# Kernel optimization log

Hardware: AMD Instinct MI355X
Metric: run time of the kernel (lower is better)

The kernel has to match this reference:

```python
import jax, jax.numpy as jnp
import numpy as np

B, S, D = 2, 2048, 768
H = 12
DK = D // H  # 64; dim_q = dim_k = dim_v
DFF = 3072
EPS = 1e-5


def layer_norm(x, w, b):
    mu = jnp.mean(x, axis=-1, keepdims=True)
    var = jnp.var(x, axis=-1, keepdims=True)
    return (x - mu) * jax.lax.rsqrt(var + EPS) * w + b


def setup_inputs() -> dict:
    key = jax.random.key(0)
    ks = jax.random.split(key, 12)
    s = 0.02
    return {
        "src": jax.random.normal(ks[0], (B, S, D), dtype=jnp.float32),
        # per-head projections stacked over heads: [H, D, DK]
        "Wq": jax.random.normal(ks[1], (H, D, DK), dtype=jnp.float32) * s,
        "bq": jnp.zeros((H, DK), dtype=jnp.float32),
        "Wk": jax.random.normal(ks[2], (H, D, DK), dtype=jnp.float32) * s,
        "bk": jnp.zeros((H, DK), dtype=jnp.float32),
        "Wv": jax.random.normal(ks[3], (H, D, DK), dtype=jnp.float32) * s,
        "bv": jnp.zeros((H, DK), dtype=jnp.float32),
        # output projection: [H*DK, D]
        "Wo": jax.random.normal(ks[4], (H * DK, D), dtype=jnp.float32) * s,
        "bo": jnp.zeros((D,), dtype=jnp.float32),
        "ln1_w": jnp.ones((D,), dtype=jnp.float32),
        "ln1_b": jnp.zeros((D,), dtype=jnp.float32),
        "W1": jax.random.normal(ks[5], (D, DFF), dtype=jnp.float32) * s,
        "b1": jnp.zeros((DFF,), dtype=jnp.float32),
        "W2": jax.random.normal(ks[6], (DFF, D), dtype=jnp.float32) * s,
        "b2": jnp.zeros((D,), dtype=jnp.float32),
        "ln2_w": jnp.ones((D,), dtype=jnp.float32),
        "ln2_b": jnp.zeros((D,), dtype=jnp.float32),
    }


def reference(src, Wq, bq, Wk, bk, Wv, bv, Wo, bo, ln1_w, ln1_b,
              W1, b1, W2, b2, ln2_w, ln2_b):
    # per-head q/k/v projections, batched over heads via einsum
    q = jnp.einsum('bsd,hdk->bhsk', src, Wq) + bq[None, :, None, :]
    k = jnp.einsum('bsd,hdk->bhsk', src, Wk) + bk[None, :, None, :]
    v = jnp.einsum('bsd,hdk->bhsk', src, Wv) + bv[None, :, None, :]
    scale = jnp.asarray(DK, src.dtype) ** 0.5
    scores = jnp.einsum('bhsk,bhtk->bhst', q, k) / scale  # [B,H,S,S]
    attn = jax.nn.softmax(scores, axis=-1)
    ctx = jnp.einsum('bhst,bhtk->bhsk', attn, v)
    # concat heads along feature dim (matches torch.cat over head outputs)
    ctx = ctx.transpose(0, 2, 1, 3).reshape(src.shape[0], src.shape[1], H * DK)
    attn_out = ctx @ Wo + bo
    x = layer_norm(src + attn_out, ln1_w, ln1_b)
    ff = jax.nn.relu(x @ W1 + b1) @ W2 + b2
    return layer_norm(x + ff, ln2_w, ln2_b)
```

## Files before the change

### kernel.cpp

```cpp
#include <hip/hip_runtime.h>
#include <hip/hip_bf16.h>

#define S_LEN 2048
#define DMODEL 768
#define NHEAD 12
#define DKH 64
#define DFF_K 3072
#define MROWS 4096

typedef __attribute__((ext_vector_type(8))) short bf16x8;
typedef __attribute__((ext_vector_type(8))) unsigned short us8;
typedef __attribute__((ext_vector_type(4))) float f32x4;

__device__ __forceinline__ float bfu2f(unsigned short u) {
  return __uint_as_float(((unsigned int)u) << 16);
}
__device__ __forceinline__ unsigned short f2bfu(float f) {
  __hip_bfloat16 h = __float2bfloat16(f);
  return *reinterpret_cast<unsigned short*>(&h);
}

__global__ __launch_bounds__(256) void convert_kernel(
    const float* __restrict__ in, unsigned short* __restrict__ out, int n4)
{
  const int i = blockIdx.x * 256 + threadIdx.x;
  if (i < n4) {
    float4 v = *(const float4*)(in + (size_t)i * 4);
    ushort4 o;
    o.x = f2bfu(v.x); o.y = f2bfu(v.y); o.z = f2bfu(v.z); o.w = f2bfu(v.w);
    *(ushort4*)(out + (size_t)i * 4) = o;
  }
}

__device__ __forceinline__ void transpose_conv_body(
    const float* in, unsigned short* out, int R, int Ctot, int head,
    int bx, int by, int tid)
{
  __shared__ float t[64][68];
  const int r0 = bx * 64;
  const int c0 = by * 64;
  const float* ib;
  int ld;
  if (head) { ib = in + (size_t)by * R * 64; ld = 64; }
  else      { ib = in + c0;                  ld = Ctot; }
  const int lr = tid >> 4;
  const int lc = (tid & 15) << 2;

#pragma unroll
  for (int rr = 0; rr < 4; ++rr) {
    const int row = rr * 16 + lr;
    float4 v = *(const float4*)(ib + (size_t)(r0 + row) * ld + lc);
    t[row][lc + 0] = v.x; t[row][lc + 1] = v.y;
    t[row][lc + 2] = v.z; t[row][lc + 3] = v.w;
  }
  __syncthreads();
#pragma unroll
  for (int rr = 0; rr < 4; ++rr) {
    const int oc = rr * 16 + lr;
    ushort4 o;
    o.x = f2bfu(t[lc + 0][oc]); o.y = f2bfu(t[lc + 1][oc]);
    o.z = f2bfu(t[lc + 2][oc]); o.w = f2bfu(t[lc + 3][oc]);
    *(ushort4*)(out + (size_t)(c0 + oc) * R + r0 + lc) = o;
  }
}

__global__ __launch_bounds__(256) void transpose_conv_kernel(
    const float* __restrict__ in, unsigned short* __restrict__ out,
    int R, int Ctot, int head)
{
  transpose_conv_body(in, out, R, Ctot, head, blockIdx.x, blockIdx.y, threadIdx.x);
}

__global__ __launch_bounds__(256) void transpose_conv4_kernel(
    const float* __restrict__ i0, const float* __restrict__ i1,
    const float* __restrict__ i2, const float* __restrict__ i3,
    unsigned short* __restrict__ o0, unsigned short* __restrict__ o1,
    unsigned short* __restrict__ o2, unsigned short* __restrict__ o3)
{
  const int z = blockIdx.z;
  const float* in = (z == 0) ? i0 : (z == 1) ? i1 : (z == 2) ? i2 : i3;
  unsigned short* out = (z == 0) ? o0 : (z == 1) ? o1 : (z == 2) ? o2 : o3;
  transpose_conv_body(in, out, DMODEL, DMODEL, (z < 3) ? 1 : 0,
                      blockIdx.x, blockIdx.y, threadIdx.x);
}

__global__ __launch_bounds__(256) void mfma_gemm_kernel(
    const unsigned short* __restrict__ A,
    const unsigned short* __restrict__ BT,
    const float* __restrict__ bias,
    unsigned short* __restrict__ C,
    int K, int N, int relu, int klen, size_t out_stride)
{
  __shared__ unsigned short As[128][40];
  __shared__ unsigned short Bs[128][40];

  const int tid  = threadIdx.x;
  const int wid  = tid >> 6;
  const int lane = tid & 63;
  const int ml   = lane & 15;
  const int quad = lane >> 4;
  const int wm   = (wid & 1) * 64;
  const int wn   = (wid >> 1) * 64;
  const int row0 = blockIdx.x * 128;
  const int col0 = blockIdx.y * 128;
  const int zed  = blockIdx.z;
  const int kb0  = zed * klen;

  const int sr = tid >> 2;
  const int sk = (tid & 3) << 3;

  f32x4 acc[4][4];
#pragma unroll
  for (int i = 0; i < 4; ++i)
#pragma unroll
    for (int j = 0; j < 4; ++j)
#pragma unroll
      for (int r = 0; r < 4; ++r) acc[i][j][r] = 0.f;

  for (int k0 = kb0; k0 < kb0 + klen; k0 += 32) {
    us8 a0 = *(const us8*)(A + (size_t)(row0 + sr) * K + k0 + sk);
    us8 a1 = *(const us8*)(A + (size_t)(row0 + sr + 64) * K + k0 + sk);
    us8 b0 = *(const us8*)(BT + (size_t)(col0 + sr) * K + k0 + sk);
    us8 b1 = *(const us8*)(BT + (size_t)(col0 + sr + 64) * K + k0 + sk);
    *(us8*)&As[sr][sk]      = a0;
    *(us8*)&As[sr + 64][sk] = a1;
    *(us8*)&Bs[sr][sk]      = b0;
    *(us8*)&Bs[sr + 64][sk] = b1;
    __syncthreads();

    bf16x8 af[4], bfr[4];
#pragma unroll
    for (int i = 0; i < 4; ++i)
      af[i] = *(const bf16x8*)&As[wm + i * 16 + ml][quad << 3];
#pragma unroll
    for (int j = 0; j < 4; ++j)
      bfr[j] = *(const bf16x8*)&Bs[wn + j * 16 + ml][quad << 3];
#pragma unroll
    for (int i = 0; i < 4; ++i)
#pragma unroll
      for (int j = 0; j < 4; ++j)
        acc[i][j] = __builtin_amdgcn_mfma_f32_16x16x32_bf16(
            af[i], bfr[j], acc[i][j], 0, 0, 0);
    __syncthreads();
  }

  unsigned short* Cz = C + (size_t)zed * out_stride;
#pragma unroll
  for (int j = 0; j < 4; ++j) {
    const int col = col0 + wn + j * 16 + ml;
    const float bb = (zed == 0) ? bias[col] : 0.f;
#pragma unroll
    for (int i = 0; i < 4; ++i) {
      const int r0g = row0 + wm + i * 16 + (quad << 2);
#pragma unroll
      for (int r = 0; r < 4; ++r) {
        float v = acc[i][j][r] + bb;
        if (relu) v = fmaxf(v, 0.f);
        Cz[(size_t)(r0g + r) * N + col] = f2bfu(v);
      }
    }
  }
}

__global__ __launch_bounds__(256) void qkv_gemm_kernel(
    const unsigned short* __restrict__ A,
    const unsigned short* __restrict__ W0, const unsigned short* __restrict__ W1,
    const unsigned short* __restrict__ W2,
    const float* __restrict__ bq, const float* __restrict__ bk,
    const float* __restrict__ bv,
    unsigned short* __restrict__ C0, unsigned short* __restrict__ C1,
    unsigned short* __restrict__ C2)
{
  __shared__ unsigned short As[128][40];
  __shared__ unsigned short Bs[128][40];
  const int z = blockIdx.z;
  const unsigned short* BT = (z == 0) ? W0 : (z == 1) ? W1 : W2;
  const float* bias = (z == 0) ? bq : (z == 1) ? bk : bv;
  unsigned short* C = (z == 0) ? C0 : (z == 1) ? C1 : C2;
  const int K = DMODEL, N = DMODEL;

  const int tid  = threadIdx.x;
  const int wid  = tid >> 6;
  const int lane = tid & 63;
  const int ml   = lane & 15;
  const int quad = lane >> 4;
  const int wm   = (wid & 1) * 64;
  const int wn   = (wid >> 1) * 64;
  const int row0 = blockIdx.x * 128;
  const int col0 = blockIdx.y * 128;
  const int sr = tid >> 2;
  const int sk = (tid & 3) << 3;

  f32x4 acc[4][4];
#pragma unroll
  for (int i = 0; i < 4; ++i)
#pragma unroll
    for (int j = 0; j < 4; ++j)
#pragma unroll
      for (int r = 0; r < 4; ++r) acc[i][j][r] = 0.f;

  for (int k0 = 0; k0 < K; k0 += 32) {
    us8 a0 = *(const us8*)(A + (size_t)(row0 + sr) * K + k0 + sk);
    us8 a1 = *(const us8*)(A + (size_t)(row0 + sr + 64) * K + k0 + sk);
    us8 b0 = *(const us8*)(BT + (size_t)(col0 + sr) * K + k0 + sk);
    us8 b1 = *(const us8*)(BT + (size_t)(col0 + sr + 64) * K + k0 + sk);
    *(us8*)&As[sr][sk]      = a0;
    *(us8*)&As[sr + 64][sk] = a1;
    *(us8*)&Bs[sr][sk]      = b0;
    *(us8*)&Bs[sr + 64][sk] = b1;
    __syncthreads();
    bf16x8 af[4], bfr[4];
#pragma unroll
    for (int i = 0; i < 4; ++i)
      af[i] = *(const bf16x8*)&As[wm + i * 16 + ml][quad << 3];
#pragma unroll
    for (int j = 0; j < 4; ++j)
      bfr[j] = *(const bf16x8*)&Bs[wn + j * 16 + ml][quad << 3];
#pragma unroll
    for (int i = 0; i < 4; ++i)
#pragma unroll
      for (int j = 0; j < 4; ++j)
        acc[i][j] = __builtin_amdgcn_mfma_f32_16x16x32_bf16(
            af[i], bfr[j], acc[i][j], 0, 0, 0);
    __syncthreads();
  }

#pragma unroll
  for (int j = 0; j < 4; ++j) {
    const int col = col0 + wn + j * 16 + ml;
    const float bb = bias[col];
#pragma unroll
    for (int i = 0; i < 4; ++i) {
      const int r0g = row0 + wm + i * 16 + (quad << 2);
      if (z == 2) {
        const int bb_ = r0g >> 11, s = r0g & 2047;
        const int hh = col >> 6, dd = col & 63;
        ushort4 o;
        o.x = f2bfu(acc[i][j][0] + bb); o.y = f2bfu(acc[i][j][1] + bb);
        o.z = f2bfu(acc[i][j][2] + bb); o.w = f2bfu(acc[i][j][3] + bb);
        *(ushort4*)(C + ((size_t)((bb_ * NHEAD + hh) * DKH + dd)) * S_LEN + s) = o;
      } else {
#pragma unroll
        for (int r = 0; r < 4; ++r)
          C[(size_t)(r0g + r) * N + col] = f2bfu(acc[i][j][r] + bb);
      }
    }
  }
}

#define FATS 72
#define SCL2E 0.1803368822f
__global__ __launch_bounds__(256) void flash_attn_mfma(
    const unsigned short* __restrict__ Q,
    const unsigned short* __restrict__ K,
    const unsigned short* __restrict__ VT,
    unsigned short* __restrict__ O)
{
  __shared__ unsigned short Ks[64][FATS];
  __shared__ unsigned short Vs[64][FATS];
  __shared__ unsigned short QP[4][16][FATS];

  const int tid  = threadIdx.x;
  const int wid  = tid >> 6;
  const int lane = tid & 63;
  const int ml   = lane & 15;
  const int quad = lane >> 4;
  const int h    = blockIdx.x, b = blockIdx.y;
  const int q0   = blockIdx.z * 64;

  const size_t qkbase = ((size_t)b * S_LEN) * DMODEL + (size_t)h * DKH;
  const size_t vtbase = ((size_t)(b * NHEAD + h)) * DKH * S_LEN;

  const int sr = tid >> 2;
  const int sc = (tid & 3) << 4;

  {
    const unsigned short* qp = Q + qkbase + (size_t)(q0 + sr) * DMODEL + sc;
    *(us8*)&QP[sr >> 4][sr & 15][sc]     = *(const us8*)qp;
    *(us8*)&QP[sr >> 4][sr & 15][sc + 8] = *(const us8*)(qp + 8);
  }
  bf16x8 qf[2];
  qf[0] = *(const bf16x8*)&QP[wid][ml][quad << 3];
  qf[1] = *(const bf16x8*)&QP[wid][ml][32 + (quad << 3)];

  float lsum = 0.f;
  f32x4 oacc[4];
#pragma unroll
  for (int dt = 0; dt < 4; ++dt)
#pragma unroll
    for (int r = 0; r < 4; ++r) oacc[dt][r] = 0.f;

  for (int kt = 0; kt < S_LEN; kt += 64) {
    __syncthreads();
    {
      const unsigned short* kp = K + qkbase + (size_t)(kt + sr) * DMODEL + sc;
      *(us8*)&Ks[sr][sc]     = *(const us8*)kp;
      *(us8*)&Ks[sr][sc + 8] = *(const us8*)(kp + 8);
      const unsigned short* vp = VT + vtbase + (size_t)sr * S_LEN + kt + sc;
      *(us8*)&Vs[sr][sc]     = *(const us8*)vp;
      *(us8*)&Vs[sr][sc + 8] = *(const us8*)(vp + 8);
    }
    __syncthreads();

    f32x4 sacc[4];
#pragma unroll
    for (int mt = 0; mt < 4; ++mt)
#pragma unroll
      for (int r = 0; r < 4; ++r) sacc[mt][r] = 0.f;
#pragma unroll
    for (int mt = 0; mt < 4; ++mt) {
      bf16x8 kf0 = *(const bf16x8*)&Ks[mt * 16 + ml][quad << 3];
      bf16x8 kf1 = *(const bf16x8*)&Ks[mt * 16 + ml][32 + (quad << 3)];
      sacc[mt] = __builtin_amdgcn_mfma_f32_16x16x32_bf16(kf0, qf[0], sacc[mt], 0, 0, 0);
      sacc[mt] = __builtin_amdgcn_mfma_f32_16x16x32_bf16(kf1, qf[1], sacc[mt], 0, 0, 0);
    }

    float p[4][4];
#pragma unroll
    for (int mt2 = 0; mt2 < 4; ++mt2)
#pragma unroll
      for (int r = 0; r < 4; ++r) {
        const float e = exp2f(sacc[mt2][r] * SCL2E);
        p[mt2][r] = e;
        lsum += e;
      }

#pragma unroll
    for (int mt2 = 0; mt2 < 4; ++mt2) {
      ushort4 o;
      o.x = f2bfu(p[mt2][0]); o.y = f2bfu(p[mt2][1]);
      o.z = f2bfu(p[mt2][2]); o.w = f2bfu(p[mt2][3]);
      *(ushort4*)&QP[wid][ml][mt2 * 16 + (quad << 2)] = o;
    }
    bf16x8 pf0 = *(const bf16x8*)&QP[wid][ml][quad << 3];
    bf16x8 pf1 = *(const bf16x8*)&QP[wid][ml][32 + (quad << 3)];

#pragma unroll
    for (int dt = 0; dt < 4; ++dt) {
      bf16x8 vf0 = *(const bf16x8*)&Vs[dt * 16 + ml][quad << 3];
      bf16x8 vf1 = *(const bf16x8*)&Vs[dt * 16 + ml][32 + (quad << 3)];
      oacc[dt] = __builtin_amdgcn_mfma_f32_16x16x32_bf16(vf0, pf0, oacc[dt], 0, 0, 0);
      oacc[dt] = __builtin_amdgcn_mfma_f32_16x16x32_bf16(vf1, pf1, oacc[dt], 0, 0, 0);
    }
  }

  lsum += __shfl_xor(lsum, 16);
  lsum += __shfl_xor(lsum, 32);
  const float inv = 1.f / lsum;
  const int qrow = q0 + wid * 16 + ml;
#pragma unroll
  for (int dt = 0; dt < 4; ++dt)
#pragma unroll
    for (int r = 0; r < 4; ++r)
      O[qkbase + (size_t)qrow * DMODEL + dt * 16 + (quad << 2) + r] =
          f2bfu(oacc[dt][r] * inv);
}

__global__ __launch_bounds__(256) void add_ln_kernel(
    const void* __restrict__ X, const void* __restrict__ Y,
    const void* __restrict__ Y2,
    const float* __restrict__ w, const float* __restrict__ bvec,
    void* __restrict__ out, int xbf, int ybf, int obf)
{
  __shared__ float buf[DMODEL];
  __shared__ float rbuf[8];
  const int tid  = threadIdx.x;
  const int lane = tid & 63, wv = tid >> 6;
  const size_t base = (size_t)blockIdx.x * DMODEL;

  float s = 0.f, s2 = 0.f;
#pragma unroll
  for (int j = tid; j < DMODEL; j += 256) {
    float xv = xbf ? bfu2f(((const unsigned short*)X)[base + j])
                   : ((const float*)X)[base + j];
    float yv = ybf ? bfu2f(((const unsigned short*)Y)[base + j])
                   : ((const float*)Y)[base + j];
    float v = xv + yv;
    if (Y2) v += ybf ? bfu2f(((const unsigned short*)Y2)[base + j])
                     : ((const float*)Y2)[base + j];
    buf[j] = v; s += v; s2 += v * v;
  }
#pragma unroll
  for (int o = 32; o; o >>= 1) { s += __shfl_xor(s, o); s2 += __shfl_xor(s2, o); }
  if (lane == 0) { rbuf[wv] = s; rbuf[4 + wv] = s2; }
  __syncthreads();
  const float S  = rbuf[0] + rbuf[1] + rbuf[2] + rbuf[3];
  const float S2 = rbuf[4] + rbuf[5] + rbuf[6] + rbuf[7];
  const float mean = S * (1.f / (float)DMODEL);
  const float var  = S2 * (1.f / (float)DMODEL) - mean * mean;
  const float rstd = rsqrtf(var + 1e-5f);
#pragma unroll
  for (int j = tid; j < DMODEL; j += 256) {
    float v = (buf[j] - mean) * rstd * w[j] + bvec[j];
    if (obf) ((unsigned short*)out)[base + j] = f2bfu(v);
    else     ((float*)out)[base + j] = v;
  }
}

extern "C" void kernel_launch(void* const* d_in, const int* in_sizes, int n_in,
                              void* d_out, int out_size, void* d_ws, size_t ws_size,
                              hipStream_t stream) {
  const float* src  = (const float*)d_in[0];
  const float* Wq   = (const float*)d_in[1];
  const float* bq   = (const float*)d_in[2];
  const float* Wk   = (const float*)d_in[3];
  const float* bk   = (const float*)d_in[4];
  const float* Wv   = (const float*)d_in[5];
  const float* bv   = (const float*)d_in[6];
  const float* Wo   = (const float*)d_in[7];
  const float* bo   = (const float*)d_in[8];
  const float* ln1w = (const float*)d_in[9];
  const float* ln1b = (const float*)d_in[10];
  const float* W1   = (const float*)d_in[11];
  const float* b1   = (const float*)d_in[12];
  const float* W2   = (const float*)d_in[13];
  const float* b2   = (const float*)d_in[14];
  const float* ln2w = (const float*)d_in[15];
  const float* ln2b = (const float*)d_in[16];
  (void)ws_size; (void)in_sizes; (void)n_in; (void)out_size;

  unsigned short* p = (unsigned short*)d_ws;
  const size_t SEG = (size_t)MROWS * DMODEL;
  unsigned short* srcb = p; p += SEG;
  unsigned short* qb   = p; p += SEG;
  unsigned short* kb_  = p; p += SEG;
  unsigned short* vbT  = p; p += SEG;
  unsigned short* ctx  = p; p += SEG;
  unsigned short* ff   = p; p += (size_t)MROWS * DFF_K;
  unsigned short* wqt  = p; p += (size_t)DMODEL * DMODEL;
  unsigned short* wkt  = p; p += (size_t)DMODEL * DMODEL;
  unsigned short* wvt  = p; p += (size_t)DMODEL * DMODEL;
  unsigned short* wot  = p; p += (size_t)DMODEL * DMODEL;
  unsigned short* w1t  = p; p += (size_t)DMODEL * DFF_K;
  unsigned short* w2t  = p; p += (size_t)DMODEL * DFF_K;
  unsigned short* x1 = kb_;

  dim3 blk(256);

  convert_kernel<<<dim3(SEG / 1024), blk, 0, stream>>>(src, srcb, (int)(SEG / 4));
  transpose_conv4_kernel<<<dim3(12, 12, 4), blk, 0, stream>>>(
      Wq, Wk, Wv, Wo, wqt, wkt, wvt, wot);
  transpose_conv_kernel<<<dim3(12, 48), blk, 0, stream>>>(W1, w1t, DMODEL, DFF_K, 0);
  transpose_conv_kernel<<<dim3(48, 12), blk, 0, stream>>>(W2, w2t, DFF_K, DMODEL, 0);

  dim3 gqkv(MROWS / 128, DMODEL / 128, 3);
  qkv_gemm_kernel<<<gqkv, blk, 0, stream>>>(srcb, wqt, wkt, wvt, bq, bk, bv,
                                            qb, kb_, vbT);

  dim3 ga(NHEAD, 2, S_LEN / 64);
  flash_attn_mfma<<<ga, blk, 0, stream>>>(qb, kb_, vbT, ctx);

  dim3 gWo(MROWS / 128, DMODEL / 128, 2);
  mfma_gemm_kernel<<<gWo, blk, 0, stream>>>(ctx, wot, bo, qb,
                                            DMODEL, DMODEL, 0, DMODEL / 2, 2 * SEG);

  add_ln_kernel<<<dim3(MROWS), blk, 0, stream>>>(srcb, qb, vbT,
                                                 ln1w, ln1b, x1, 1, 1, 1);

  dim3 gF1(MROWS / 128, DFF_K / 128, 1);
  mfma_gemm_kernel<<<gF1, blk, 0, stream>>>(x1, w1t, b1, ff,
                                            DMODEL, DFF_K, 1, DMODEL, 0);

  dim3 gW2(MROWS / 128, DMODEL / 128, 2);
  mfma_gemm_kernel<<<gW2, blk, 0, stream>>>(ff, w2t, b2, qb,
                                            DFF_K, DMODEL, 0, DFF_K / 2, 2 * SEG);

  add_ln_kernel<<<dim3(MROWS), blk, 0, stream>>>(x1, qb, vbT,
                                                 ln2w, ln2b, (float*)d_out, 1, 1, 0);
}
```

Baseline: 335.8 us.

## Prefetch next K-tile into registers and use narrower N tiles for small GEMMs

The GEMM and flash-attention kernels now issue the global loads for the next K/V or K-slice tile into registers before running the MFMAs on the current tile, so memory latency overlaps with compute. The GEMM kernel is templated on its N-tile width, and the QKV, Wo and W2 GEMMs switch to 64-wide column tiles, doubling their block counts to fill the GPU's compute units better. This costs extra live registers for the prefetched data, and the narrower tiles reuse each loaded A tile across fewer columns.

```diff
diff --git a/kernel.cpp b/kernel.cpp
--- a/kernel.cpp
+++ b/kernel.cpp
@@ -84,6 +84,7 @@
                       blockIdx.x, blockIdx.y, threadIdx.x);
 }
 
+template<int BN>
 __global__ __launch_bounds__(256) void mfma_gemm_kernel(
     const unsigned short* __restrict__ A,
     const unsigned short* __restrict__ BT,
@@ -91,8 +92,10 @@
     unsigned short* __restrict__ C,
     int K, int N, int relu, int klen, size_t out_stride)
 {
+  constexpr int WN = (BN == 128) ? 64 : 32;
+  constexpr int NJ = WN / 16;
   __shared__ unsigned short As[128][40];
-  __shared__ unsigned short Bs[128][40];
+  __shared__ unsigned short Bs[BN][40];
 
   const int tid  = threadIdx.x;
   const int wid  = tid >> 6;
@@ -100,45 +103,61 @@
   const int ml   = lane & 15;
   const int quad = lane >> 4;
   const int wm   = (wid & 1) * 64;
-  const int wn   = (wid >> 1) * 64;
+  const int wn   = (wid >> 1) * WN;
   const int row0 = blockIdx.x * 128;
-  const int col0 = blockIdx.y * 128;
+  const int col0 = blockIdx.y * BN;
   const int zed  = blockIdx.z;
   const int kb0  = zed * klen;
+  const int kend = kb0 + klen;
 
   const int sr = tid >> 2;
   const int sk = (tid & 3) << 3;
 
-  f32x4 acc[4][4];
+  const unsigned short* pA0 = A  + (size_t)(row0 + sr) * K + sk;
+  const unsigned short* pA1 = A  + (size_t)(row0 + sr + 64) * K + sk;
+  const unsigned short* pB0 = BT + (size_t)(col0 + sr) * K + sk;
+  const unsigned short* pB1 = BT + (size_t)(col0 + sr + 64) * K + sk;
+
+  f32x4 acc[4][NJ];
 #pragma unroll
   for (int i = 0; i < 4; ++i)
 #pragma unroll
-    for (int j = 0; j < 4; ++j)
+    for (int j = 0; j < NJ; ++j)
 #pragma unroll
       for (int r = 0; r < 4; ++r) acc[i][j][r] = 0.f;
 
-  for (int k0 = kb0; k0 < kb0 + klen; k0 += 32) {
-    us8 a0 = *(const us8*)(A + (size_t)(row0 + sr) * K + k0 + sk);
-    us8 a1 = *(const us8*)(A + (size_t)(row0 + sr + 64) * K + k0 + sk);
-    us8 b0 = *(const us8*)(BT + (size_t)(col0 + sr) * K + k0 + sk);
-    us8 b1 = *(const us8*)(BT + (size_t)(col0 + sr + 64) * K + k0 + sk);
-    *(us8*)&As[sr][sk]      = a0;
-    *(us8*)&As[sr + 64][sk] = a1;
-    *(us8*)&Bs[sr][sk]      = b0;
-    *(us8*)&Bs[sr + 64][sk] = b1;
+  us8 ra0 = *(const us8*)(pA0 + kb0);
+  us8 ra1 = *(const us8*)(pA1 + kb0);
+  us8 rb0 = *(const us8*)(pB0 + kb0);
+  us8 rb1;
+  if (BN == 128) rb1 = *(const us8*)(pB1 + kb0);
+
+  for (int k0 = kb0; k0 < kend; k0 += 32) {
+    *(us8*)&As[sr][sk]      = ra0;
+    *(us8*)&As[sr + 64][sk] = ra1;
+    *(us8*)&Bs[sr][sk]      = rb0;
+    if (BN == 128) *(us8*)&Bs[sr + 64][sk] = rb1;
     __syncthreads();
 
-    bf16x8 af[4], bfr[4];
+    const int kn = k0 + 32;
+    if (kn < kend) {
+      ra0 = *(const us8*)(pA0 + kn);
+      ra1 = *(const us8*)(pA1 + kn);
+      rb0 = *(const us8*)(pB0 + kn);
+      if (BN == 128) rb1 = *(const us8*)(pB1 + kn);
+    }
+
+    bf16x8 af[4], bfr[NJ];
 #pragma unroll
     for (int i = 0; i < 4; ++i)
       af[i] = *(const bf16x8*)&As[wm + i * 16 + ml][quad << 3];
 #pragma unroll
-    for (int j = 0; j < 4; ++j)
+    for (int j = 0; j < NJ; ++j)
       bfr[j] = *(const bf16x8*)&Bs[wn + j * 16 + ml][quad << 3];
 #pragma unroll
     for (int i = 0; i < 4; ++i)
 #pragma unroll
-      for (int j = 0; j < 4; ++j)
+      for (int j = 0; j < NJ; ++j)
         acc[i][j] = __builtin_amdgcn_mfma_f32_16x16x32_bf16(
             af[i], bfr[j], acc[i][j], 0, 0, 0);
     __syncthreads();
@@ -146,7 +165,7 @@
 
   unsigned short* Cz = C + (size_t)zed * out_stride;
 #pragma unroll
-  for (int j = 0; j < 4; ++j) {
+  for (int j = 0; j < NJ; ++j) {
     const int col = col0 + wn + j * 16 + ml;
     const float bb = (zed == 0) ? bias[col] : 0.f;
 #pragma unroll
@@ -172,7 +191,7 @@
     unsigned short* __restrict__ C2)
 {
   __shared__ unsigned short As[128][40];
-  __shared__ unsigned short Bs[128][40];
+  __shared__ unsigned short Bs[64][40];
   const int z = blockIdx.z;
   const unsigned short* BT = (z == 0) ? W0 : (z == 1) ? W1 : W2;
   const float* bias = (z == 0) ? bq : (z == 1) ? bk : bv;
@@ -185,48 +204,59 @@
   const int ml   = lane & 15;
   const int quad = lane >> 4;
   const int wm   = (wid & 1) * 64;
-  const int wn   = (wid >> 1) * 64;
+  const int wn   = (wid >> 1) * 32;
   const int row0 = blockIdx.x * 128;
-  const int col0 = blockIdx.y * 128;
+  const int col0 = blockIdx.y * 64;
   const int sr = tid >> 2;
   const int sk = (tid & 3) << 3;
 
-  f32x4 acc[4][4];
+  const unsigned short* pA0 = A  + (size_t)(row0 + sr) * K + sk;
+  const unsigned short* pA1 = A  + (size_t)(row0 + sr + 64) * K + sk;
+  const unsigned short* pB0 = BT + (size_t)(col0 + sr) * K + sk;
+
+  f32x4 acc[4][2];
 #pragma unroll
   for (int i = 0; i < 4; ++i)
 #pragma unroll
-    for (int j = 0; j < 4; ++j)
+    for (int j = 0; j < 2; ++j)
 #pragma unroll
       for (int r = 0; r < 4; ++r) acc[i][j][r] = 0.f;
 
+  us8 ra0 = *(const us8*)pA0;
+  us8 ra1 = *(const us8*)pA1;
+  us8 rb0 = *(const us8*)pB0;
+
   for (int k0 = 0; k0 < K; k0 += 32) {
-    us8 a0 = *(const us8*)(A + (size_t)(row0 + sr) * K + k0 + sk);
-    us8 a1 = *(const us8*)(A + (size_t)(row0 + sr + 64) * K + k0 + sk);
-    us8 b0 = *(const us8*)(BT + (size_t)(col0 + sr) * K + k0 + sk);
-    us8 b1 = *(const us8*)(BT + (size_t)(col0 + sr + 64) * K + k0 + sk);
-    *(us8*)&As[sr][sk]      = a0;
-    *(us8*)&As[sr + 64][sk] = a1;
-    *(us8*)&Bs[sr][sk]      = b0;
-    *(us8*)&Bs[sr + 64][sk] = b1;
+    *(us8*)&As[sr][sk]      = ra0;
+    *(us8*)&As[sr + 64][sk] = ra1;
+    *(us8*)&Bs[sr][sk]      = rb0;
     __syncthreads();
-    bf16x8 af[4], bfr[4];
+
+    const int kn = k0 + 32;
+    if (kn < K) {
+      ra0 = *(const us8*)(pA0 + kn);
+      ra1 = *(const us8*)(pA1 + kn);
+      rb0 = *(const us8*)(pB0 + kn);
+    }
+
+    bf16x8 af[4], bfr[2];
 #pragma unroll
     for (int i = 0; i < 4; ++i)
       af[i] = *(const bf16x8*)&As[wm + i * 16 + ml][quad << 3];
 #pragma unroll
-    for (int j = 0; j < 4; ++j)
+    for (int j = 0; j < 2; ++j)
       bfr[j] = *(const bf16x8*)&Bs[wn + j * 16 + ml][quad << 3];
 #pragma unroll
     for (int i = 0; i < 4; ++i)
 #pragma unroll
-      for (int j = 0; j < 4; ++j)
+      for (int j = 0; j < 2; ++j)
         acc[i][j] = __builtin_amdgcn_mfma_f32_16x16x32_bf16(
             af[i], bfr[j], acc[i][j], 0, 0, 0);
     __syncthreads();
   }
 
 #pragma unroll
-  for (int j = 0; j < 4; ++j) {
+  for (int j = 0; j < 2; ++j) {
     const int col = col0 + wn + j * 16 + ml;
     const float bb = bias[col];
 #pragma unroll
@@ -283,6 +313,9 @@
   qf[0] = *(const bf16x8*)&QP[wid][ml][quad << 3];
   qf[1] = *(const bf16x8*)&QP[wid][ml][32 + (quad << 3)];
 
+  const unsigned short* pK = K + qkbase + (size_t)sr * DMODEL + sc;
+  const unsigned short* pV = VT + vtbase + (size_t)sr * S_LEN + sc;
+
   float lsum = 0.f;
   f32x4 oacc[4];
 #pragma unroll
@@ -290,17 +323,26 @@
 #pragma unroll
     for (int r = 0; r < 4; ++r) oacc[dt][r] = 0.f;
 
+  us8 rk0 = *(const us8*)(pK);
+  us8 rk1 = *(const us8*)(pK + 8);
+  us8 rv0 = *(const us8*)(pV);
+  us8 rv1 = *(const us8*)(pV + 8);
+
   for (int kt = 0; kt < S_LEN; kt += 64) {
     __syncthreads();
-    {
-      const unsigned short* kp = K + qkbase + (size_t)(kt + sr) * DMODEL + sc;
-      *(us8*)&Ks[sr][sc]     = *(const us8*)kp;
-      *(us8*)&Ks[sr][sc + 8] = *(const us8*)(kp + 8);
-      const unsigned short* vp = VT + vtbase + (size_t)sr * S_LEN + kt + sc;
-      *(us8*)&Vs[sr][sc]     = *(const us8*)vp;
-      *(us8*)&Vs[sr][sc + 8] = *(const us8*)(vp + 8);
-    }
+    *(us8*)&Ks[sr][sc]     = rk0;
+    *(us8*)&Ks[sr][sc + 8] = rk1;
+    *(us8*)&Vs[sr][sc]     = rv0;
+    *(us8*)&Vs[sr][sc + 8] = rv1;
     __syncthreads();
+
+    const int ktn = kt + 64;
+    if (ktn < S_LEN) {
+      rk0 = *(const us8*)(pK + (size_t)ktn * DMODEL);
+      rk1 = *(const us8*)(pK + (size_t)ktn * DMODEL + 8);
+      rv0 = *(const us8*)(pV + ktn);
+      rv1 = *(const us8*)(pV + ktn + 8);
+    }
 
     f32x4 sacc[4];
 #pragma unroll
@@ -443,27 +485,27 @@
   transpose_conv_kernel<<<dim3(12, 48), blk, 0, stream>>>(W1, w1t, DMODEL, DFF_K, 0);
   transpose_conv_kernel<<<dim3(48, 12), blk, 0, stream>>>(W2, w2t, DFF_K, DMODEL, 0);
 
-  dim3 gqkv(MROWS / 128, DMODEL / 128, 3);
+  dim3 gqkv(MROWS / 128, DMODEL / 64, 3);
   qkv_gemm_kernel<<<gqkv, blk, 0, stream>>>(srcb, wqt, wkt, wvt, bq, bk, bv,
                                             qb, kb_, vbT);
 
   dim3 ga(NHEAD, 2, S_LEN / 64);
   flash_attn_mfma<<<ga, blk, 0, stream>>>(qb, kb_, vbT, ctx);
 
-  dim3 gWo(MROWS / 128, DMODEL / 128, 2);
-  mfma_gemm_kernel<<<gWo, blk, 0, stream>>>(ctx, wot, bo, qb,
-                                            DMODEL, DMODEL, 0, DMODEL / 2, 2 * SEG);
+  dim3 gWo(MROWS / 128, DMODEL / 64, 2);
+  mfma_gemm_kernel<64><<<gWo, blk, 0, stream>>>(ctx, wot, bo, qb,
+                                                DMODEL, DMODEL, 0, DMODEL / 2, 2 * SEG);
 
   add_ln_kernel<<<dim3(MROWS), blk, 0, stream>>>(srcb, qb, vbT,
                                                  ln1w, ln1b, x1, 1, 1, 1);
 
   dim3 gF1(MROWS / 128, DFF_K / 128, 1);
-  mfma_gemm_kernel<<<gF1, blk, 0, stream>>>(x1, w1t, b1, ff,
-                                            DMODEL, DFF_K, 1, DMODEL, 0);
-
-  dim3 gW2(MROWS / 128, DMODEL / 128, 2);
-  mfma_gemm_kernel<<<gW2, blk, 0, stream>>>(ff, w2t, b2, qb,
-                                            DFF_K, DMODEL, 0, DFF_K / 2, 2 * SEG);
+  mfma_gemm_kernel<128><<<gF1, blk, 0, stream>>>(x1, w1t, b1, ff,
+                                                 DMODEL, DFF_K, 1, DMODEL, 0);
+
+  dim3 gW2(MROWS / 128, DMODEL / 64, 2);
+  mfma_gemm_kernel<64><<<gW2, blk, 0, stream>>>(ff, w2t, b2, qb,
+                                                DFF_K, DMODEL, 0, DFF_K / 2, 2 * SEG);
 
   add_ln_kernel<<<dim3(MROWS), blk, 0, stream>>>(x1, qb, vbT,
                                                  ln2w, ln2b, (float*)d_out, 1, 1, 0);
```

Result: faster. 305.5 us (-9.0%).
